# Kernel tuning notes

Measured on AMD Instinct MI355X. Metric: run time of the kernel, lower is better.

## Reference

```python
import jax, jax.numpy as jnp
import numpy as np

B, T, H, W = 2, 8, 14, 14
S = H * W
DIM, HEADS = 768, 12
HD = DIM // HEADS  # 64


def setup_inputs() -> dict:
    key = jax.random.key(0)
    ks = jax.random.split(key, 6)
    std = 0.02
    return {
        "x": jax.random.normal(ks[0], (B, T, S, DIM), jnp.float32),
        "qkv_w": jax.random.normal(ks[1], (3 * DIM, DIM), jnp.float32) * std,
        "proj_w": jax.random.normal(ks[2], (DIM, DIM), jnp.float32) * std,
        "proj_b": jnp.zeros((DIM,), jnp.float32),
        "rel_pos_h": jax.random.normal(ks[3], (2 * H - 1, HD), jnp.float32) * std,
        "rel_pos_w": jax.random.normal(ks[4], (2 * W - 1, HD), jnp.float32) * std,
        "rel_pos_t": jax.random.normal(ks[5], (2 * T - 1, HD), jnp.float32) * std,
    }


def _rel_table(rel_pos, q_len):
    # q_len == k_len here, so get_rel_pos is identity and indices simplify
    idx = np.arange(q_len)[:, None] - np.arange(q_len)[None, :] + (q_len - 1)
    return rel_pos[idx]  # [q_len, k_len, head_dim]


def reference(x, qkv_w, proj_w, proj_b, rel_pos_h, rel_pos_w, rel_pos_t):
    B_, T_, S_, C = x.shape
    H_ = W_ = int(S_ ** 0.5)
    N = T_ * S_
    hd = C // HEADS
    scale = hd ** -0.5

    xf = x.reshape(B_, N, C)
    qkv = (xf @ qkv_w.T).reshape(B_, N, 3, HEADS, hd).transpose(2, 0, 3, 1, 4)
    q, k, v = qkv[0], qkv[1], qkv[2]  # each [B, heads, N, hd]

    attn = jnp.einsum('bhqd,bhkd->bhqk', q, k) * scale  # [B, heads, N, N]

    # Decomposed relative-position bias (note: uses UNscaled q, as in original)
    r_q = q.reshape(B_, HEADS, T_, H_, W_, hd)
    Rh = _rel_table(rel_pos_h, H_)  # [H, H, hd]
    Rw = _rel_table(rel_pos_w, W_)  # [W, W, hd]
    Rt = _rel_table(rel_pos_t, T_)  # [T, T, hd]
    rel_h = jnp.einsum('bythwc,hkc->bythwk', r_q, Rh)
    rel_w = jnp.einsum('bythwc,wkc->bythwk', r_q, Rw)
    rel_t = jnp.einsum('bythwc,tkc->bythwk', r_q, Rt)

    attn = (attn.reshape(B_, HEADS, T_, H_, W_, T_, H_, W_)
            + rel_h[:, :, :, :, :, None, :, None]
            + rel_w[:, :, :, :, :, None, None, :]
            + rel_t[:, :, :, :, :, :, None, None]
            ).reshape(B_, HEADS, N, N)

    attn = jax.nn.softmax(attn, axis=-1)
    out = jnp.einsum('bhqk,bhkd->bhqd', attn, v)  # [B, heads, N, hd]
    out = out.transpose(0, 2, 1, 3).reshape(B_, N, C)
    out = out @ proj_w.T + proj_b
    return out.reshape(B_, T_, S_, C)
```

## Files before the change

### kernel.cpp

```cpp
#include <hip/hip_runtime.h>

using f16   = _Float16;
using f16x4 = __attribute__((ext_vector_type(4))) _Float16;
using f16x8 = __attribute__((ext_vector_type(8))) _Float16;
using f32x4 = __attribute__((ext_vector_type(4))) float;
using u32x4 = __attribute__((ext_vector_type(4))) unsigned int;
using fp16x2_raw = __fp16 __attribute__((ext_vector_type(2)));

#define MFMA16(a, b, c) __builtin_amdgcn_mfma_f32_16x16x32_f16((a), (b), (c), 0, 0, 0)

namespace {
constexpr int kT = 8, kWd = 14, kS = 196;
constexpr int kN = 1568;
constexpr int kM = 3136;
constexpr int kHeads = 12;
constexpr int kNp = 1664;
constexpr float kLog2e = 1.4426950408889634f;
constexpr size_t OFF_Q    = 4718592;
constexpr size_t OFF_KF   = 14942208;
constexpr size_t OFF_KONE = 20054016;
constexpr size_t OFF_VSWZ = 20267008;
constexpr size_t WS_TOTAL = 25378816;
constexpr int kKoneTot = 13 * 8 * 2 * 64 * 8;

__device__ inline f16x4 pack4(float4 v) {
  union { fp16x2_raw h2[2]; f16x4 f4; } u;
  u.h2[0] = __builtin_amdgcn_cvt_pkrtz(v.x, v.y);
  u.h2[1] = __builtin_amdgcn_cvt_pkrtz(v.z, v.w);
  return u.f4;
}

__device__ inline float fast_exp2(float x) {
#if __has_builtin(__builtin_amdgcn_exp2f)
  return __builtin_amdgcn_exp2f(x);
#else
  return __expf(x * 0.6931471805599453f);
#endif
}

__device__ inline void gload_lds16(const f16* g, f16* l) {
  __builtin_amdgcn_global_load_lds(
      (const __attribute__((address_space(1))) unsigned int*)g,
      (__attribute__((address_space(3))) unsigned int*)l,
      16, 0, 0);
}

__device__ inline float dotqLDS(const f16x8* qh, const f16* Rrow) {
  float s = 0.f;
#pragma unroll
  for (int i = 0; i < 8; ++i) {
    f16x8 a = qh[i];
    f16x8 b = *(const f16x8*)(Rrow + i * 8);
#pragma unroll
    for (int k = 0; k < 8; ++k) s += (float)a[k] * (float)b[k];
  }
  return s;
}
}

__global__ __launch_bounds__(256, 2) void arp_gemm_qkv(
    const float* __restrict__ X, const float* __restrict__ qkvw,
    f16* __restrict__ qf, f16* __restrict__ kfrag, f16* __restrict__ vswz,
    f16* __restrict__ konefrag) {
  __shared__ char smem[34816];
  f16* sA = (f16*)smem;
  f16* sB = (f16*)(smem + 10240);
  f16* sE = (f16*)smem;
  const int tid = threadIdx.x, lane = tid & 63, wv = tid >> 6;

  {
    int g = (blockIdx.y * 18 + blockIdx.x) * 256 + tid;
    if (g < kKoneTot) {
      int j = g & 7;
      int ln = (g >> 3) & 63;
      int s2 = (g >> 9) & 1;
      int nt = (g >> 10) & 7;
      int kt = g >> 13;
      int slot = ln & 15, qd = ln >> 4;
      int kin = (nt >> 1) * 32 + (slot >> 2) * 8 + (nt & 1) * 4 + (slot & 3);
      int key = kt * 128 + kin;
      int c = s2 * 32 + qd * 8 + j;
      int t2 = key / kS; int rm = key - t2 * kS;
      int h2 = rm / kWd; int w2 = rm - h2 * kWd;
      if (t2 > kT - 1) t2 = kT - 1;
      float v = 0.f;
      if (c == h2) v = 1.f;
      else if (c == 14 + w2) v = 1.f;
      else if (c == 28 + t2) v = 1.f;
      else if (c == 36 && key >= kN) v = 1.f;
      konefrag[g] = (f16)v;
    }
  }

  int orig = blockIdx.y * 18 + blockIdx.x;
  int xcd = orig & 7;
  int base = (xcd < 2) ? xcd * 57 : 2 * 57 + (xcd - 2) * 56;
  int wgid = base + (orig >> 3);
  const int m0 = (wgid / 18) * 128, n0 = (wgid % 18) * 128;

  const int wm = (wv & 1) * 64, wn = (wv >> 1) * 64;
  const int frow = lane & 15, quad = lane >> 4, fcol = quad * 8;
  const f32x4 vzero = {0.f, 0.f, 0.f, 0.f};
  f32x4 acc[4][4];
#pragma unroll
  for (int i = 0; i < 4; ++i)
#pragma unroll
    for (int j = 0; j < 4; ++j) acc[i][j] = vzero;

  float4 pA[2][2], pB[2][2];
#pragma unroll
  for (int i = 0; i < 2; ++i) {
    int idx = i * 256 + tid;
    int r = idx >> 2, c8 = (idx & 3) * 8;
    int gm = m0 + r; if (gm >= kM) gm = kM - 1;
    pA[i][0] = *(const float4*)(X + (size_t)gm * 768 + c8);
    pA[i][1] = *(const float4*)(X + (size_t)gm * 768 + c8 + 4);
    pB[i][0] = *(const float4*)(qkvw + (size_t)(n0 + r) * 768 + c8);
    pB[i][1] = *(const float4*)(qkvw + (size_t)(n0 + r) * 768 + c8 + 4);
  }

  for (int kt = 0; kt < 24; ++kt) {
#pragma unroll
    for (int i = 0; i < 2; ++i) {
      int idx = i * 256 + tid;
      int r = idx >> 2, c8 = (idx & 3) * 8;
      union { f16x4 h[2]; u32x4 u; } ua, ub;
      ua.h[0] = pack4(pA[i][0]); ua.h[1] = pack4(pA[i][1]);
      ub.h[0] = pack4(pB[i][0]); ub.h[1] = pack4(pB[i][1]);
      *(u32x4*)&sA[r * 40 + c8] = ua.u;
      *(u32x4*)&sB[r * 40 + c8] = ub.u;
    }
    __syncthreads();
    if (kt < 23) {
      int ko = (kt + 1) * 32;
#pragma unroll
      for (int i = 0; i < 2; ++i) {
        int idx = i * 256 + tid;
        int r = idx >> 2, c8 = (idx & 3) * 8;
        int gm = m0 + r; if (gm >= kM) gm = kM - 1;
        pA[i][0] = *(const float4*)(X + (size_t)gm * 768 + ko + c8);
        pA[i][1] = *(const float4*)(X + (size_t)gm * 768 + ko + c8 + 4);
        pB[i][0] = *(const float4*)(qkvw + (size_t)(n0 + r) * 768 + ko + c8);
        pB[i][1] = *(const float4*)(qkvw + (size_t)(n0 + r) * 768 + ko + c8 + 4);
      }
    }
    f16x8 af[4], bf[4];
#pragma unroll
    for (int t = 0; t < 4; ++t) {
      af[t] = *(const f16x8*)&sA[(wm + t * 16 + frow) * 40 + fcol];
      bf[t] = *(const f16x8*)&sB[(wn + t * 16 + frow) * 40 + fcol];
    }
#pragma unroll
    for (int mt = 0; mt < 4; ++mt)
#pragma unroll
      for (int nt = 0; nt < 4; ++nt)
        acc[mt][nt] = MFMA16(af[mt], bf[nt], acc[mt][nt]);
    __syncthreads();
  }

  const int which = n0 / 768;
  if (which == 2) {
#pragma unroll
    for (int mt = 0; mt < 4; ++mt)
#pragma unroll
      for (int nt = 0; nt < 4; ++nt) {
        int cl = wn + nt * 16 + frow;
#pragma unroll
        for (int rg = 0; rg < 4; ++rg) {
          int rl = wm + mt * 16 + quad * 4 + rg;
          sE[cl * 136 + rl] = (f16)acc[mt][nt][rg];
        }
      }
    __syncthreads();
    int cl = tid >> 1;
    int rb = (tid & 1) * 64;
    int rem = n0 + cl - 1536;
    int hh = rem >> 6, d = rem & 63;
    int td = d >> 4, fr = d & 15;
#pragma unroll
    for (int j = 0; j < 8; ++j) {
      int ms = m0 + rb + j * 8;
      if (ms < kM) {
        int bb2 = (ms >= kN) ? 1 : 0;
        int ns = ms - bb2 * kN;
        int bh = bb2 * kHeads + hh;
        int kt2 = ns >> 7, kr = ns & 127;
        int kc = kr >> 5, qd = (kr >> 3) & 3;
        f16* dst = vswz + ((((size_t)(bh * 13 + kt2)) * 4 + td) * 4 + kc) * 512
                        + (qd * 16 + fr) * 8;
        *(u32x4*)dst = *(const u32x4*)&sE[cl * 136 + rb + j * 8];
      }
    }
  } else {
#pragma unroll
    for (int mt = 0; mt < 4; ++mt) {
      int rbase = m0 + wm + mt * 16 + quad * 4;
#pragma unroll
      for (int nt = 0; nt < 4; ++nt) {
        int col0 = n0 + wn + nt * 16;
        int rem = col0 - which * 768;
        int hh = rem >> 6;
        int d = (rem & 63) + frow;
        int s = d >> 5, qd2 = (d >> 3) & 3, j = d & 7;
#pragma unroll
        for (int rg = 0; rg < 4; ++rg) {
          int m = rbase + rg;
          if (m < kM) {
            int bb2 = (m >= kN) ? 1 : 0;
            int ns = m - bb2 * kN;
            int bh = bb2 * kHeads + hh;
            float av = acc[mt][nt][rg];
            if (which == 0) {
              av *= kLog2e;
              qf[((size_t)bh * kNp + ns) * 64 + d] = (f16)av;
            } else {
              av *= 0.125f;
              int kt2 = ns >> 7;
              int kin = ns & 127;
              int nt2 = ((kin >> 5) << 1) | ((kin >> 2) & 1);
              int slot = ((kin >> 3) & 3) * 4 + (kin & 3);
              kfrag[(((size_t)(bh * 13 + kt2) * 8 + nt2) * 2 + s) * 512
                    + (qd2 * 16 + slot) * 8 + j] = (f16)av;
            }
          }
        }
      }
    }
  }
}

__global__ __launch_bounds__(256, 3) void arp_attn(
    const f16* qf,
    const float* __restrict__ Rh, const float* __restrict__ Rw, const float* __restrict__ Rt,
    const f16* __restrict__ kfrag, const f16* __restrict__ konefrag,
    const f16* __restrict__ vswz, f16* qfO) {
  __shared__ char pool[49152];
  f16* sKa = (f16*)pool;
  f16* sKb = (f16*)(pool + 16384);
  f16* sV  = (f16*)(pool + 32768);
  f16* sQE = (f16*)pool;
  f16* sR  = (f16*)(pool + 8192);

  const int tid = threadIdx.x, lane = tid & 63, wv = tid >> 6;
  const int Lb  = blockIdx.y * 25 + blockIdx.x;
  const int Lw  = (Lb & 7) * 75 + (Lb >> 3);
  const int q0 = (Lw % 25) * 64;
  const int bh = Lw / 25;
  const int frow = lane & 15, quad = lane >> 4;
  const f32x4 vzero = {0.f, 0.f, 0.f, 0.f};

  const f16* kba = kfrag + (size_t)bh * 13 * 8192;
  const f16* vba = vswz + (size_t)bh * 13 * 8192;

  for (int g = tid; g < 69 * 16; g += 256) {
    int row = g >> 4, c4 = (g & 15) * 4;
    const float* src = (row < 27) ? Rh + row * 64 + c4
                     : (row < 54) ? Rw + (row - 27) * 64 + c4
                                  : Rt + (row - 54) * 64 + c4;
    *(f16x4*)&sR[row * 72 + c4] = pack4(*(const float4*)src);
  }
  __syncthreads();

  {
    int q = q0 + lane;
    int qc = (q < kN) ? q : kN - 1;
    int tq = qc / kS, sr = qc - tq * kS;
    int hq = sr / kWd, wq = sr - hq * kWd;
    if (wv < 3) {
      f16x8 qh[8];
      const f16x8* qv8 = (const f16x8*)(qf + ((size_t)bh * kNp + q) * 64);
#pragma unroll
      for (int i = 0; i < 8; ++i) qh[i] = qv8[i];
      if (wv == 0) {
#pragma unroll
        for (int e = 0; e < 14; ++e)
          sQE[lane * 64 + e] = (f16)dotqLDS(qh, &sR[(hq - e + 13) * 72]);
      } else if (wv == 1) {
#pragma unroll
        for (int e = 0; e < 14; ++e)
          sQE[lane * 64 + 14 + e] = (f16)dotqLDS(qh, &sR[(wq - e + 40) * 72]);
      } else {
#pragma unroll
        for (int e = 0; e < 8; ++e)
          sQE[lane * 64 + 28 + e] = (f16)dotqLDS(qh, &sR[(tq - e + 61) * 72]);
      }
    } else {
      sQE[lane * 64 + 36] = (f16)(-30000.f);
#pragma unroll
      for (int e = 37; e < 64; ++e) sQE[lane * 64 + e] = (f16)0.f;
    }
  }
  __syncthreads();

  f16x8 aQ0, aQ1, aQE0, aQE1;
  {
    int row = q0 + wv * 16 + frow;
    const f16* qp = qf + ((size_t)bh * kNp + row) * 64;
    aQ0 = *(const f16x8*)(qp + quad * 8);
    aQ1 = *(const f16x8*)(qp + 32 + quad * 8);
    int rl = wv * 16 + frow;
    aQE0 = *(const f16x8*)&sQE[rl * 64 + quad * 8];
    aQE1 = *(const f16x8*)&sQE[rl * 64 + 32 + quad * 8];
  }
  __syncthreads();

#pragma unroll
  for (int i = 0; i < 4; ++i) {
    int u = (i * 256 + tid) * 8;
    gload_lds16(kba + u, sKa + u);
    gload_lds16(konefrag + u, sKb + u);
    gload_lds16(vba + u, sV + u);
  }

  float den = 0.f;
  f32x4 Oc[4];
#pragma unroll
  for (int t = 0; t < 4; ++t) Oc[t] = vzero;

  for (int kt = 0; kt < 13; ++kt) {
    __syncthreads();

    f32x4 Sc[8];
    __builtin_amdgcn_s_setprio(1);
#pragma unroll
    for (int nt = 0; nt < 8; ++nt) {
      const f16* ka = &sKa[nt * 1024 + lane * 8];
      const f16* kb = &sKb[nt * 1024 + lane * 8];
      f32x4 s = MFMA16(*(const f16x8*)(ka), aQ0, vzero);
      s = MFMA16(*(const f16x8*)(ka + 512), aQ1, s);
      s = MFMA16(*(const f16x8*)(kb), aQE0, s);
      Sc[nt] = MFMA16(*(const f16x8*)(kb + 512), aQE1, s);
    }
    __builtin_amdgcn_s_setprio(0);
    f16x8 bV[4][4];
#pragma unroll
    for (int td = 0; td < 4; ++td)
#pragma unroll
      for (int kc = 0; kc < 4; ++kc)
        bV[td][kc] = *(const f16x8*)&sV[(td * 4 + kc) * 512 + lane * 8];
    __syncthreads();

    if (kt < 12) {
      const f16* kfa = kba + (size_t)(kt + 1) * 8192;
      const f16* koa = konefrag + (size_t)(kt + 1) * 8192;
      const f16* vfa = vba + (size_t)(kt + 1) * 8192;
#pragma unroll
      for (int i = 0; i < 4; ++i) {
        int u = (i * 256 + tid) * 8;
        gload_lds16(kfa + u, sKa + u);
        gload_lds16(koa + u, sKb + u);
        gload_lds16(vfa + u, sV + u);
      }
    }

#pragma unroll
    for (int nt = 0; nt < 8; ++nt)
#pragma unroll
      for (int r = 0; r < 4; ++r)
        Sc[nt][r] = fast_exp2(Sc[nt][r]);

    __builtin_amdgcn_s_setprio(1);
#pragma unroll
    for (int kc = 0; kc < 4; ++kc) {
      union { _Float16 h[8]; f16x8 v; } up;
#pragma unroll
      for (int r = 0; r < 4; ++r) {
        up.h[r]     = (f16)Sc[2 * kc][r];
        up.h[4 + r] = (f16)Sc[2 * kc + 1][r];
      }
#pragma unroll
      for (int r = 0; r < 4; ++r)
        den += (float)up.h[r] + (float)up.h[4 + r];
#pragma unroll
      for (int td = 0; td < 4; ++td)
        Oc[td] = MFMA16(up.v, bV[td][kc], Oc[td]);
    }
    __builtin_amdgcn_s_setprio(0);
  }

  den += __shfl_xor(den, 16, 64);
  den += __shfl_xor(den, 32, 64);
  float lr[4];
#pragma unroll
  for (int r = 0; r < 4; ++r)
    lr[r] = 1.f / __shfl(den, quad * 4 + r, 64);
#pragma unroll
  for (int td = 0; td < 4; ++td)
#pragma unroll
    for (int r = 0; r < 4; ++r) {
      int row = q0 + wv * 16 + quad * 4 + r;
      if (row < kN) {
        float val = Oc[td][r] * lr[r];
        qfO[((size_t)bh * kNp + row) * 64 + td * 16 + frow] = (f16)val;
      }
    }
}

__global__ __launch_bounds__(256, 4) void arp_gemm_proj(
    const f16* A, const float* __restrict__ projw,
    const float* __restrict__ bias, float* __restrict__ out) {
  __shared__ f16 sA[64 * 40];
  __shared__ f16 sB[64 * 40];
  const int tid = threadIdx.x, lane = tid & 63, wv = tid >> 6;

  int orig = blockIdx.y * 12 + blockIdx.x;
  int xcd = orig & 7;
  int base = (xcd < 4) ? xcd * 74 : 4 * 74 + (xcd - 4) * 73;
  int wgid = base + (orig >> 3);
  const int m0 = (wgid / 12) * 64, n0 = (wgid % 12) * 64;

  const int frow = lane & 15, quad = lane >> 4, fcol = quad * 8;
  const f32x4 vzero = {0.f, 0.f, 0.f, 0.f};
  f32x4 acc[4];
#pragma unroll
  for (int j = 0; j < 4; ++j) acc[j] = vzero;

  u32x4 pA;
  float4 pB[2];
  {
    int r = tid >> 2, c8 = (tid & 3) * 8;
    int m = m0 + r;
    int bb = (m >= kN) ? 1 : 0;
    int ns = m - bb * kN;
    pA = *(const u32x4*)(A + ((size_t)(bb * kHeads) * kNp + ns) * 64 + c8);
    pB[0] = *(const float4*)(projw + (size_t)(n0 + r) * 768 + c8);
    pB[1] = *(const float4*)(projw + (size_t)(n0 + r) * 768 + c8 + 4);
  }

  for (int kt = 0; kt < 24; ++kt) {
    {
      int r = tid >> 2, c8 = (tid & 3) * 8;
      *(u32x4*)&sA[r * 40 + c8] = pA;
      union { f16x4 h[2]; u32x4 u; } ub;
      ub.h[0] = pack4(pB[0]); ub.h[1] = pack4(pB[1]);
      *(u32x4*)&sB[r * 40 + c8] = ub.u;
    }
    __syncthreads();
    if (kt < 23) {
      int k1 = kt + 1;
      int hd = k1 >> 1, dof = (k1 & 1) * 32;
      int r = tid >> 2, c8 = (tid & 3) * 8;
      int m = m0 + r;
      int bb = (m >= kN) ? 1 : 0;
      int ns = m - bb * kN;
      pA = *(const u32x4*)(A + ((size_t)(bb * kHeads + hd) * kNp + ns) * 64 + dof + c8);
      pB[0] = *(const float4*)(projw + (size_t)(n0 + r) * 768 + k1 * 32 + c8);
      pB[1] = *(const float4*)(projw + (size_t)(n0 + r) * 768 + k1 * 32 + c8 + 4);
    }
    f16x8 af = *(const f16x8*)&sA[(wv * 16 + frow) * 40 + fcol];
    f16x8 bf[4];
#pragma unroll
    for (int u = 0; u < 4; ++u)
      bf[u] = *(const f16x8*)&sB[(u * 16 + frow) * 40 + fcol];
#pragma unroll
    for (int u = 0; u < 4; ++u)
      acc[u] = MFMA16(af, bf[u], acc[u]);
    __syncthreads();
  }
#pragma unroll
  for (int u = 0; u < 4; ++u) {
    int col = n0 + u * 16 + frow;
    float bv = bias[col];
#pragma unroll
    for (int rg = 0; rg < 4; ++rg) {
      int m = m0 + wv * 16 + quad * 4 + rg;
      out[(size_t)m * 768 + col] = acc[u][rg] + bv;
    }
  }
}

extern "C" void kernel_launch(void* const* d_in, const int* in_sizes, int n_in,
                              void* d_out, int out_size, void* d_ws, size_t ws_size,
                              hipStream_t stream) {
  if (ws_size < WS_TOTAL) return;
  const float* x      = (const float*)d_in[0];
  const float* qkv_w  = (const float*)d_in[1];
  const float* proj_w = (const float*)d_in[2];
  const float* proj_b = (const float*)d_in[3];
  const float* rph    = (const float*)d_in[4];
  const float* rpw    = (const float*)d_in[5];
  const float* rpt    = (const float*)d_in[6];
  char* ws = (char*)d_ws;
  f16* qf       = (f16*)(ws + OFF_Q);
  f16* kfrag    = (f16*)(ws + OFF_KF);
  f16* konefrag = (f16*)(ws + OFF_KONE);
  f16* vswz     = (f16*)(ws + OFF_VSWZ);

  arp_gemm_qkv<<<dim3(18, 25), 256, 0, stream>>>(x, qkv_w, qf, kfrag, vswz, konefrag);
  arp_attn<<<dim3(25, 24), 256, 0, stream>>>(qf, rph, rpw, rpt, kfrag, konefrag, vswz, qf);
  arp_gemm_proj<<<dim3(12, 49), 256, 0, stream>>>(qf, proj_w, proj_b, (float*)d_out);
}
```

Measured before the change: 161.3 us.

## Double-buffer half-size key/value tiles in attention loop with one barrier

Splits each 128-key tile into two 64-key halves and ping-pongs them between two 24KB LDS buffers. The next half-tile is prefetched at the top of each iteration, which removes the second barrier per iteration and overlaps the global-to-LDS copy with the current compute. The cost is twice as many loop iterations and barriers overall, plus more address arithmetic for the strided V loads. LDS use stays at 48KB.

```diff
diff --git a/kernel.cpp b/kernel.cpp
--- a/kernel.cpp
+++ b/kernel.cpp
@@ -235,9 +235,6 @@
     const f16* __restrict__ kfrag, const f16* __restrict__ konefrag,
     const f16* __restrict__ vswz, f16* qfO) {
   __shared__ char pool[49152];
-  f16* sKa = (f16*)pool;
-  f16* sKb = (f16*)(pool + 16384);
-  f16* sV  = (f16*)(pool + 32768);
   f16* sQE = (f16*)pool;
   f16* sR  = (f16*)(pool + 8192);
 
@@ -304,12 +301,20 @@
   }
   __syncthreads();
 
-#pragma unroll
-  for (int i = 0; i < 4; ++i) {
-    int u = (i * 256 + tid) * 8;
-    gload_lds16(kba + u, sKa + u);
-    gload_lds16(konefrag + u, sKb + u);
-    gload_lds16(vba + u, sV + u);
+  {
+    f16* dst = (f16*)pool;
+#pragma unroll
+    for (int i = 0; i < 6; ++i) {
+      int u = i * 256 + tid;
+      const f16* src;
+      if (u < 512)       src = kba + u * 8;
+      else if (u < 1024) src = konefrag + (u - 512) * 8;
+      else {
+        int v2 = u - 1024;
+        src = vba + (v2 >> 7) * 2048 + (v2 & 127) * 8;
+      }
+      gload_lds16(src, dst + u * 8);
+    }
   }
 
   float den = 0.f;
@@ -317,63 +322,73 @@
 #pragma unroll
   for (int t = 0; t < 4; ++t) Oc[t] = vzero;
 
-  for (int kt = 0; kt < 13; ++kt) {
+  for (int ht = 0; ht < 26; ++ht) {
     __syncthreads();
 
-    f32x4 Sc[8];
+    if (ht < 25) {
+      int h1 = (ht + 1) & 1;
+      const f16* kfa = kba + (size_t)((ht + 1) >> 1) * 8192 + h1 * 4096;
+      const f16* koa = konefrag + (size_t)((ht + 1) >> 1) * 8192 + h1 * 4096;
+      const f16* vfa = vba + (size_t)((ht + 1) >> 1) * 8192;
+      f16* dst = (f16*)(pool + h1 * 24576);
+#pragma unroll
+      for (int i = 0; i < 6; ++i) {
+        int u = i * 256 + tid;
+        const f16* src;
+        if (u < 512)       src = kfa + u * 8;
+        else if (u < 1024) src = koa + (u - 512) * 8;
+        else {
+          int v2 = u - 1024;
+          src = vfa + (v2 >> 7) * 2048 + h1 * 1024 + (v2 & 127) * 8;
+        }
+        gload_lds16(src, dst + u * 8);
+      }
+    }
+
+    const f16* bKa = (const f16*)(pool + (ht & 1) * 24576);
+    const f16* bKb = bKa + 4096;
+    const f16* bVv = bKa + 8192;
+
+    f32x4 Sc[4];
     __builtin_amdgcn_s_setprio(1);
 #pragma unroll
-    for (int nt = 0; nt < 8; ++nt) {
-      const f16* ka = &sKa[nt * 1024 + lane * 8];
-      const f16* kb = &sKb[nt * 1024 + lane * 8];
+    for (int ntl = 0; ntl < 4; ++ntl) {
+      const f16* ka = &bKa[ntl * 1024 + lane * 8];
+      const f16* kb = &bKb[ntl * 1024 + lane * 8];
       f32x4 s = MFMA16(*(const f16x8*)(ka), aQ0, vzero);
       s = MFMA16(*(const f16x8*)(ka + 512), aQ1, s);
       s = MFMA16(*(const f16x8*)(kb), aQE0, s);
-      Sc[nt] = MFMA16(*(const f16x8*)(kb + 512), aQE1, s);
+      Sc[ntl] = MFMA16(*(const f16x8*)(kb + 512), aQE1, s);
     }
     __builtin_amdgcn_s_setprio(0);
-    f16x8 bV[4][4];
+    f16x8 bV[4][2];
 #pragma unroll
     for (int td = 0; td < 4; ++td)
 #pragma unroll
-      for (int kc = 0; kc < 4; ++kc)
-        bV[td][kc] = *(const f16x8*)&sV[(td * 4 + kc) * 512 + lane * 8];
-    __syncthreads();
-
-    if (kt < 12) {
-      const f16* kfa = kba + (size_t)(kt + 1) * 8192;
-      const f16* koa = konefrag + (size_t)(kt + 1) * 8192;
-      const f16* vfa = vba + (size_t)(kt + 1) * 8192;
-#pragma unroll
-      for (int i = 0; i < 4; ++i) {
-        int u = (i * 256 + tid) * 8;
-        gload_lds16(kfa + u, sKa + u);
-        gload_lds16(koa + u, sKb + u);
-        gload_lds16(vfa + u, sV + u);
-      }
-    }
-
-#pragma unroll
-    for (int nt = 0; nt < 8; ++nt)
+      for (int kcl = 0; kcl < 2; ++kcl)
+        bV[td][kcl] = *(const f16x8*)&bVv[(td * 2 + kcl) * 512 + lane * 8];
+
+#pragma unroll
+    for (int ntl = 0; ntl < 4; ++ntl)
 #pragma unroll
       for (int r = 0; r < 4; ++r)
-        Sc[nt][r] = fast_exp2(Sc[nt][r]);
+        Sc[ntl][r] = fast_exp2(Sc[ntl][r]);
 
     __builtin_amdgcn_s_setprio(1);
 #pragma unroll
-    for (int kc = 0; kc < 4; ++kc) {
+    for (int kcl = 0; kcl < 2; ++kcl) {
       union { _Float16 h[8]; f16x8 v; } up;
 #pragma unroll
       for (int r = 0; r < 4; ++r) {
-        up.h[r]     = (f16)Sc[2 * kc][r];
-        up.h[4 + r] = (f16)Sc[2 * kc + 1][r];
+        up.h[r]     = (f16)Sc[2 * kcl][r];
+        up.h[4 + r] = (f16)Sc[2 * kcl + 1][r];
       }
 #pragma unroll
       for (int r = 0; r < 4; ++r)
         den += (float)up.h[r] + (float)up.h[4 + r];
 #pragma unroll
       for (int td = 0; td < 4; ++td)
-        Oc[td] = MFMA16(up.v, bV[td][kc], Oc[td]);
+        Oc[td] = MFMA16(up.v, bV[td][kcl], Oc[td]);
     }
     __builtin_amdgcn_s_setprio(0);
   }
```

After: 166.2 us. +3.0%, slower.
